# Kernel tuning notes

Measured on AMD Instinct MI355X. Metric: run time of the kernel, lower is better.

The kernel has to match this reference:

```python
import jax, jax.numpy as jnp
import numpy as np

B, S, H, HEADS = 4, 2048, 512, 8
DK = H // HEADS
LN_EPS = 1e-5
NEG_INF = -1e30


def setup_inputs() -> dict:
    key = jax.random.key(0)
    k = jax.random.split(key, 6)
    x = jax.random.normal(k[0], (B, S, H), dtype=jnp.float32)
    mask = jax.random.randint(k[1], (B, S), 0, 2, dtype=jnp.int32)
    # per-head Q/K/V projection weights stacked: [heads, H, dk]
    Wq = jax.random.normal(k[2], (HEADS, H, DK), dtype=jnp.float32) * 0.05
    Wk = jax.random.normal(k[3], (HEADS, H, DK), dtype=jnp.float32) * 0.05
    Wv = jax.random.normal(k[4], (HEADS, H, DK), dtype=jnp.float32) * 0.05
    # output projection: [heads*dk, H] (y = h @ Wo)
    Wo = jax.random.normal(k[5], (HEADS * DK, H), dtype=jnp.float32) * 0.05
    gamma = jnp.ones((H,), dtype=jnp.float32)
    beta = jnp.zeros((H,), dtype=jnp.float32)
    return {"x": x, "mask": mask, "Wq": Wq, "Wk": Wk, "Wv": Wv,
            "Wo": Wo, "gamma": gamma, "beta": beta}


def reference(x, mask, Wq, Wk, Wv, Wo, gamma, beta):
    # LayerNorm over hidden dim
    mu = jnp.mean(x, axis=-1, keepdims=True)
    var = jnp.mean(jnp.square(x - mu), axis=-1, keepdims=True)
    xn = (x - mu) * jax.lax.rsqrt(var + LN_EPS) * gamma + beta  # [B,S,H]

    mf = mask.astype(jnp.float32)  # [B,S]

    # batched per-head projections (original loops over heads)
    q = jnp.einsum('bsh,nhd->bnsd', xn, Wq)  # [B,heads,S,dk]
    kk = jnp.einsum('bsh,nhd->bnsd', xn, Wk)
    v = jnp.einsum('bsh,nhd->bnsd', xn, Wv)

    scores = jnp.einsum('bnqd,bnkd->bnqk', q, kk) / np.sqrt(DK).astype(np.float32)
    m = mf[:, None, None, :]  # [B,1,1,S] broadcast over query dim
    logits = m * scores + (1.0 - m) * NEG_INF
    probs = jax.nn.softmax(logits, axis=-1)
    attn = jnp.einsum('bnqk,bnkd->bnqd', probs, v)  # [B,heads,S,dk]

    h = attn.transpose(0, 2, 1, 3).reshape(x.shape[0], x.shape[1], HEADS * DK)
    out = h @ Wo + xn          # residual adds post-norm x (as in original)
    out = out * mf[:, :, None]  # zero out masked positions
    return out
```

## Files before the change

kernel.cpp:

```cpp
#include <hip/hip_runtime.h>
#include <hip/hip_bf16.h>
#include <math.h>

#define B_ 4
#define S_ 2048
#define H_ 512
#define HEADS_ 8
#define DK_ 64
#define NROWS_ (B_*S_)
#define LN_EPS_ 1e-5f
#define NEG_INF_ -1e30f
#define QSCALE_ (0.125f * 1.44269504088896f)

typedef short s8v __attribute__((ext_vector_type(8)));
typedef short s4v __attribute__((ext_vector_type(4)));
typedef float f4v __attribute__((ext_vector_type(4)));

__device__ __forceinline__ unsigned short f2bf(float f) {
    unsigned int u = __float_as_uint(f);
    u += 0x7FFFu + ((u >> 16) & 1u);
    return (unsigned short)(u >> 16);
}

__device__ __forceinline__ s4v pk4bf(float a, float b, float c, float d) {
    union { __hip_bfloat162 h[2]; s4v v; } u;
    u.h[0] = __float22bfloat162_rn(float2{a, b});
    u.h[1] = __float22bfloat162_rn(float2{c, d});
    return u.v;
}

__global__ __launch_bounds__(256) void wt_kernel(
        const float* __restrict__ Wq, const float* __restrict__ Wk,
        const float* __restrict__ Wv, const float* __restrict__ Wo,
        unsigned short* __restrict__ Wt) {
    __shared__ float tile[32][33];
    int z = blockIdx.z;
    int k0 = blockIdx.y * 32, c0 = blockIdx.x * 32;
    const float* src;
    int ld, drow;
    float scale = 1.f;
    if (z < 24) {
        if (blockIdx.x >= 2) return;
        int zw = z >> 3, head = z & 7;
        const float* W = (zw == 0) ? Wq : (zw == 1) ? Wk : Wv;
        if (zw == 0) scale = QSCALE_;
        src = W + (size_t)head * H_ * DK_;
        ld = DK_;
        drow = zw * 512 + head * 64;
    } else {
        src = Wo; ld = H_; drow = 1536;
    }
    int tx = threadIdx.x & 31, ty = threadIdx.x >> 5;
    #pragma unroll
    for (int i = 0; i < 4; i++)
        tile[ty * 4 + i][tx] = src[(size_t)(k0 + ty * 4 + i) * ld + c0 + tx];
    __syncthreads();
    #pragma unroll
    for (int i = 0; i < 4; i++) {
        int cc = ty * 4 + i;
        Wt[(size_t)(drow + c0 + cc) * 512 + k0 + tx] = f2bf(tile[tx][cc] * scale);
    }
}

__global__ __launch_bounds__(256) void ln_kernel(
        const float* __restrict__ x, const float* __restrict__ gamma,
        const float* __restrict__ beta, float* __restrict__ xn,
        unsigned short* __restrict__ xnb) {
    int row  = blockIdx.x * 4 + (threadIdx.x >> 6);
    int lane = threadIdx.x & 63;
    const float4* xr = (const float4*)(x + (size_t)row * H_ + lane * 8);
    float4 a = xr[0], d = xr[1];
    float s  = (a.x + a.y) + (a.z + a.w) + (d.x + d.y) + (d.z + d.w);
    float ss = (a.x*a.x + a.y*a.y) + (a.z*a.z + a.w*a.w)
             + (d.x*d.x + d.y*d.y) + (d.z*d.z + d.w*d.w);
    #pragma unroll
    for (int i = 1; i < 64; i <<= 1) {
        s  += __shfl_xor(s, i, 64);
        ss += __shfl_xor(ss, i, 64);
    }
    float mu  = s * (1.f / 512.f);
    float var = ss * (1.f / 512.f) - mu * mu;
    float rstd = rsqrtf(var + LN_EPS_);
    const float4* gp = (const float4*)(gamma + lane * 8);
    const float4* bp = (const float4*)(beta + lane * 8);
    float4 g0 = gp[0], g1 = gp[1], b0 = bp[0], b1 = bp[1];
    float4 y0, y1;
    y0.x = (a.x - mu) * rstd * g0.x + b0.x;
    y0.y = (a.y - mu) * rstd * g0.y + b0.y;
    y0.z = (a.z - mu) * rstd * g0.z + b0.z;
    y0.w = (a.w - mu) * rstd * g0.w + b0.w;
    y1.x = (d.x - mu) * rstd * g1.x + b1.x;
    y1.y = (d.y - mu) * rstd * g1.y + b1.y;
    y1.z = (d.z - mu) * rstd * g1.z + b1.z;
    y1.w = (d.w - mu) * rstd * g1.w + b1.w;
    float4* xo = (float4*)(xn + (size_t)row * H_ + lane * 8);
    xo[0] = y0; xo[1] = y1;
    union { s4v h[2]; s8v v; } pk;
    pk.h[0] = pk4bf(y0.x, y0.y, y0.z, y0.w);
    pk.h[1] = pk4bf(y1.x, y1.y, y1.z, y1.w);
    *(s8v*)(xnb + (size_t)row * H_ + lane * 8) = pk.v;
}

#define BK_ 32
__device__ __forceinline__ void gemm_tile(
        const unsigned short* __restrict__ A,
        const unsigned short* __restrict__ Bt,
        int r0, int j0, f4v acc[4][4]) {
    __shared__ unsigned short As[128][BK_ + 8];
    __shared__ unsigned short Bs[128][BK_ + 8];
    int t = threadIdx.x;
    int wv = t >> 6, L = t & 63, c = L & 15, g = L >> 4;
    int m_base = (wv & 1) * 64, n_base = (wv >> 1) * 64;
    #pragma unroll
    for (int i = 0; i < 4; i++)
        #pragma unroll
        for (int j = 0; j < 4; j++) acc[i][j] = (f4v){0.f, 0.f, 0.f, 0.f};
    for (int k0 = 0; k0 < 512; k0 += BK_) {
        __syncthreads();
        #pragma unroll
        for (int i = 0; i < 2; i++) {
            int idx = t + i * 256;
            int m = idx >> 2, k8 = idx & 3;
            s8v va = *(const s8v*)(A  + (size_t)(r0 + m) * 512 + k0 + k8 * 8);
            s8v vb = *(const s8v*)(Bt + (size_t)(j0 + m) * 512 + k0 + k8 * 8);
            *(s8v*)(&As[m][k8 * 8]) = va;
            *(s8v*)(&Bs[m][k8 * 8]) = vb;
        }
        __syncthreads();
        s8v a[4], b[4];
        #pragma unroll
        for (int i = 0; i < 4; i++)
            a[i] = *(const s8v*)(&As[m_base + i * 16 + c][g * 8]);
        #pragma unroll
        for (int j = 0; j < 4; j++)
            b[j] = *(const s8v*)(&Bs[n_base + j * 16 + c][g * 8]);
        #pragma unroll
        for (int i = 0; i < 4; i++)
            #pragma unroll
            for (int j = 0; j < 4; j++)
                acc[i][j] = __builtin_amdgcn_mfma_f32_16x16x32_bf16(
                    a[i], b[j], acc[i][j], 0, 0, 0);
    }
}

__global__ __launch_bounds__(256) void qkv_gemm(
        const unsigned short* __restrict__ xnb,
        const unsigned short* __restrict__ Wt,
        unsigned short* __restrict__ Qb, unsigned short* __restrict__ Kf,
        unsigned short* __restrict__ Vf) {
    f4v acc[4][4];
    int t = threadIdx.x;
    int wv = t >> 6, L = t & 63, c = L & 15, g = L >> 4;
    int rb = wv & 1, cb = wv >> 1;
    if (blockIdx.x < 8) {
        int m0 = blockIdx.x * 128, n0 = blockIdx.y * 128;
        gemm_tile(Wt, xnb, m0, n0, acc);
        int R0 = m0 + rb * 64;
        int C0 = n0 + cb * 64;
        int hd = (R0 >> 6) & 7;
        int b  = C0 >> 11, srow0 = C0 & 2047;
        size_t bhbase = (size_t)(b * HEADS_ + hd) * S_ * DK_;
        if (R0 < 512) {
            #pragma unroll
            for (int msub = 0; msub < 4; msub++) {
                int dk4 = msub * 16 + g * 4;
                #pragma unroll
                for (int nsub = 0; nsub < 4; nsub++) {
                    int tok = srow0 + nsub * 16 + c;
                    s4v v = pk4bf(acc[msub][nsub][0], acc[msub][nsub][1],
                                  acc[msub][nsub][2], acc[msub][nsub][3]);
                    *(s4v*)(Qb + bhbase + (size_t)tok * DK_ + dk4) = v;
                }
            }
        } else {
            unsigned short* dst = Kf + bhbase + (size_t)(srow0 >> 6) * 4096;
            #pragma unroll
            for (int msub = 0; msub < 4; msub++) {
                int gx = (msub & 1) * 2 + (g >> 1);
                int slotbase = (g & 1) * 4 + (msub >> 1) * 8;
                #pragma unroll
                for (int nsub = 0; nsub < 4; nsub++) {
                    s4v v = pk4bf(acc[msub][nsub][0], acc[msub][nsub][1],
                                  acc[msub][nsub][2], acc[msub][nsub][3]);
                    *(s4v*)(dst + nsub * 1024 + (gx * 16 + c) * 16 + slotbase) = v;
                }
            }
        }
    } else {
        int r0 = blockIdx.y * 128, j0 = 1024 + (blockIdx.x - 8) * 128;
        gemm_tile(xnb, Wt, r0, j0, acc);
        int R0 = r0 + rb * 64;
        int C0 = j0 + cb * 64;
        int hd = (C0 >> 6) & 7;
        int b = R0 >> 11, srow0 = R0 & 2047;
        unsigned short* dst = Vf + (size_t)(b * HEADS_ + hd) * S_ * DK_
                              + (size_t)(srow0 >> 6) * 4096;
        #pragma unroll
        for (int msub = 0; msub < 4; msub++)
            #pragma unroll
            for (int nsub = 0; nsub < 4; nsub++) {
                s4v v = pk4bf(acc[msub][nsub][0], acc[msub][nsub][1],
                              acc[msub][nsub][2], acc[msub][nsub][3]);
                *(s4v*)(dst + nsub * 1024 + (g * 16 + c) * 16 + msub * 4) = v;
            }
    }
}

__global__ __launch_bounds__(256, 3) void attn_kernel(
        const unsigned short* __restrict__ Qb,
        const unsigned short* __restrict__ Kf,
        const unsigned short* __restrict__ Vf,
        const int* __restrict__ mask,
        unsigned short* __restrict__ hb) {
    __shared__ float red[2][64][2][17];

    int wv   = threadIdx.x >> 6;
    int qsub = wv & 1;
    int kp   = wv >> 1;
    int L  = threadIdx.x & 63;
    int c  = L & 15;
    int g  = L >> 4;
    int bh = blockIdx.y;
    int b  = bh >> 3, n = bh & 7;
    int q0 = blockIdx.x * 64 + qsub * 32;

    const unsigned short* Qbase = Qb + (size_t)bh * S_ * DK_;
    const unsigned short* Kp = Kf + (size_t)bh * S_ * DK_ + (size_t)kp * 16 * 4096 + L * 16;
    const unsigned short* Vp = Vf + (size_t)bh * S_ * DK_ + (size_t)kp * 16 * 4096 + L * 16;
    const int* mrow = mask + b * S_ + kp * 1024;

    s8v qfA0 = *(const s8v*)(Qbase + (size_t)(q0 + c) * DK_ + g * 8);
    s8v qfA1 = *(const s8v*)(Qbase + (size_t)(q0 + c) * DK_ + 32 + g * 8);
    s8v qfB0 = *(const s8v*)(Qbase + (size_t)(q0 + 16 + c) * DK_ + g * 8);
    s8v qfB1 = *(const s8v*)(Qbase + (size_t)(q0 + 16 + c) * DK_ + 32 + g * 8);

    f4v accA[4], accB[4];
    #pragma unroll
    for (int i = 0; i < 4; i++) {
        accA[i] = (f4v){0.f, 0.f, 0.f, 0.f};
        accB[i] = (f4v){0.f, 0.f, 0.f, 0.f};
    }
    float lacA[4] = {0.f, 0.f, 0.f, 0.f};
    float lacB[4] = {0.f, 0.f, 0.f, 0.f};

    for (int kb = 0; kb < 16; kb++) {
        const unsigned short* Kn = Kp + (size_t)kb * 4096;
        const unsigned short* Vn = Vp + (size_t)kb * 4096;
        #pragma unroll
        for (int h = 0; h < 2; h++) {
            s8v k0lo = *(const s8v*)(Kn + (h * 2 + 0) * 1024);
            s8v k0hi = *(const s8v*)(Kn + (h * 2 + 0) * 1024 + 8);
            s8v k1lo = *(const s8v*)(Kn + (h * 2 + 1) * 1024);
            s8v k1hi = *(const s8v*)(Kn + (h * 2 + 1) * 1024 + 8);
            int4 mk0 = *(const int4*)(mrow + kb * 64 + h * 32 + g * 4);
            int4 mk1 = *(const int4*)(mrow + kb * 64 + h * 32 + 16 + g * 4);
            s8v vv[4];
            #pragma unroll
            for (int ds = 0; ds < 4; ds++)
                vv[ds] = *(const s8v*)(Vn + ds * 1024 + h * 8);
            f4v sA0 = (f4v){0.f,0.f,0.f,0.f}, sA1 = (f4v){0.f,0.f,0.f,0.f};
            f4v sB0 = (f4v){0.f,0.f,0.f,0.f}, sB1 = (f4v){0.f,0.f,0.f,0.f};
            sA0 = __builtin_amdgcn_mfma_f32_16x16x32_bf16(k0lo, qfA0, sA0, 0, 0, 0);
            sA0 = __builtin_amdgcn_mfma_f32_16x16x32_bf16(k0hi, qfA1, sA0, 0, 0, 0);
            sA1 = __builtin_amdgcn_mfma_f32_16x16x32_bf16(k1lo, qfA0, sA1, 0, 0, 0);
            sA1 = __builtin_amdgcn_mfma_f32_16x16x32_bf16(k1hi, qfA1, sA1, 0, 0, 0);
            sB0 = __builtin_amdgcn_mfma_f32_16x16x32_bf16(k0lo, qfB0, sB0, 0, 0, 0);
            sB0 = __builtin_amdgcn_mfma_f32_16x16x32_bf16(k0hi, qfB1, sB0, 0, 0, 0);
            sB1 = __builtin_amdgcn_mfma_f32_16x16x32_bf16(k1lo, qfB0, sB1, 0, 0, 0);
            sB1 = __builtin_amdgcn_mfma_f32_16x16x32_bf16(k1hi, qfB1, sB1, 0, 0, 0);
            float pA0[4], pA1[4], pB0[4], pB1[4];
            #pragma unroll
            for (int r = 0; r < 4; r++) {
                int m0 = (&mk0.x)[r], m1 = (&mk1.x)[r];
                pA0[r] = __builtin_amdgcn_exp2f(m0 ? sA0[r] : NEG_INF_);
                pA1[r] = __builtin_amdgcn_exp2f(m1 ? sA1[r] : NEG_INF_);
                pB0[r] = __builtin_amdgcn_exp2f(m0 ? sB0[r] : NEG_INF_);
                pB1[r] = __builtin_amdgcn_exp2f(m1 ? sB1[r] : NEG_INF_);
                lacA[r] += pA0[r] + pA1[r];
                lacB[r] += pB0[r] + pB1[r];
            }
            s4v pfA0 = pk4bf(pA0[0], pA0[1], pA0[2], pA0[3]);
            s4v pfA1 = pk4bf(pA1[0], pA1[1], pA1[2], pA1[3]);
            s4v pfB0 = pk4bf(pB0[0], pB0[1], pB0[2], pB0[3]);
            s4v pfB1 = pk4bf(pB1[0], pB1[1], pB1[2], pB1[3]);
            #pragma unroll
            for (int ds = 0; ds < 4; ds++) {
                s4v v0 = __builtin_shufflevector(vv[ds], vv[ds], 0, 1, 2, 3);
                s4v v1 = __builtin_shufflevector(vv[ds], vv[ds], 4, 5, 6, 7);
                accA[ds] = __builtin_amdgcn_mfma_f32_16x16x16bf16_1k(v0, pfA0, accA[ds], 0, 0, 0);
                accA[ds] = __builtin_amdgcn_mfma_f32_16x16x16bf16_1k(v1, pfA1, accA[ds], 0, 0, 0);
                accB[ds] = __builtin_amdgcn_mfma_f32_16x16x16bf16_1k(v0, pfB0, accB[ds], 0, 0, 0);
                accB[ds] = __builtin_amdgcn_mfma_f32_16x16x16bf16_1k(v1, pfB1, accB[ds], 0, 0, 0);
            }
        }
    }

    float lA = (lacA[0] + lacA[1]) + (lacA[2] + lacA[3]);
    float lB = (lacB[0] + lacB[1]) + (lacB[2] + lacB[3]);
    lA += __shfl_xor(lA, 16, 64);
    lA += __shfl_xor(lA, 32, 64);
    lB += __shfl_xor(lB, 16, 64);
    lB += __shfl_xor(lB, 32, 64);

    if (kp == 1) {
        #pragma unroll
        for (int d = 0; d < 4; d++) {
            #pragma unroll
            for (int r = 0; r < 4; r++) {
                red[qsub][L][0][d * 4 + r] = accA[d][r];
                red[qsub][L][1][d * 4 + r] = accB[d][r];
            }
        }
        red[qsub][L][0][16] = lA;
        red[qsub][L][1][16] = lB;
    }
    __syncthreads();
    if (kp == 0) {
        const float* srcA = &red[qsub][L][0][0];
        const float* srcB = &red[qsub][L][1][0];
        float invA = 1.f / (lA + srcA[16]);
        float invB = 1.f / (lB + srcB[16]);
        unsigned short* hpA = hb + (size_t)(b * S_ + q0 + c) * H_ + n * DK_ + g * 4;
        unsigned short* hpB = hpA + (size_t)16 * H_;
        #pragma unroll
        for (int ds = 0; ds < 4; ds++) {
            s4v oA = pk4bf((accA[ds][0] + srcA[ds * 4 + 0]) * invA,
                           (accA[ds][1] + srcA[ds * 4 + 1]) * invA,
                           (accA[ds][2] + srcA[ds * 4 + 2]) * invA,
                           (accA[ds][3] + srcA[ds * 4 + 3]) * invA);
            *(s4v*)(hpA + ds * 16) = oA;
            s4v oB = pk4bf((accB[ds][0] + srcB[ds * 4 + 0]) * invB,
                           (accB[ds][1] + srcB[ds * 4 + 1]) * invB,
                           (accB[ds][2] + srcB[ds * 4 + 2]) * invB,
                           (accB[ds][3] + srcB[ds * 4 + 3]) * invB);
            *(s4v*)(hpB + ds * 16) = oB;
        }
    }
}

__global__ __launch_bounds__(256) void out_gemm(
        const unsigned short* __restrict__ hb,
        const unsigned short* __restrict__ Wot,
        const float* __restrict__ xn, const int* __restrict__ mask,
        float* __restrict__ out) {
    f4v acc[4][4];
    int r0 = blockIdx.y * 128, j0 = blockIdx.x * 128;
    gemm_tile(hb, Wot, r0, j0, acc);
    int t = threadIdx.x;
    int wv = t >> 6, L = t & 63, c = L & 15, g = L >> 4;
    int mrow = r0 + (wv & 1) * 64 + g * 4;
    int ncol = j0 + (wv >> 1) * 64 + c;
    #pragma unroll
    for (int msub = 0; msub < 4; msub++) {
        #pragma unroll
        for (int rr = 0; rr < 4; rr++) {
            int row = mrow + msub * 16 + rr;
            float mf = (float)mask[row];
            #pragma unroll
            for (int nsub = 0; nsub < 4; nsub++) {
                int col = ncol + nsub * 16;
                size_t o = (size_t)row * H_ + col;
                out[o] = (acc[msub][nsub][rr] + xn[o]) * mf;
            }
        }
    }
}

extern "C" void kernel_launch(void* const* d_in, const int* in_sizes, int n_in,
                              void* d_out, int out_size, void* d_ws, size_t ws_size,
                              hipStream_t stream) {
    const float* x     = (const float*)d_in[0];
    const int*   mask  = (const int*)d_in[1];
    const float* Wq    = (const float*)d_in[2];
    const float* Wk    = (const float*)d_in[3];
    const float* Wv    = (const float*)d_in[4];
    const float* Wo    = (const float*)d_in[5];
    const float* gamma = (const float*)d_in[6];
    const float* beta  = (const float*)d_in[7];
    float* out = (float*)d_out;

    size_t nelem = (size_t)NROWS_ * H_;
    char* ws = (char*)d_ws;
    float*          xn  = (float*)ws;          ws += nelem * 4;
    unsigned short* xnb = (unsigned short*)ws; ws += nelem * 2;
    unsigned short* hb  = (unsigned short*)ws; ws += nelem * 2;
    unsigned short* Qb  = (unsigned short*)ws; ws += nelem * 2;
    unsigned short* Kf  = (unsigned short*)ws; ws += nelem * 2;
    unsigned short* Vf  = (unsigned short*)ws; ws += nelem * 2;
    unsigned short* Wt  = (unsigned short*)ws;

    wt_kernel<<<dim3(16, 16, 25), 256, 0, stream>>>(Wq, Wk, Wv, Wo, Wt);
    ln_kernel<<<NROWS_ / 4, 256, 0, stream>>>(x, gamma, beta, xn, xnb);
    qkv_gemm<<<dim3(12, 64), 256, 0, stream>>>(xnb, Wt, Qb, Kf, Vf);
    attn_kernel<<<dim3(S_ / 64, B_ * HEADS_), 256, 0, stream>>>(
        Qb, Kf, Vf, mask, hb);
    out_gemm<<<dim3(4, 64), 256, 0, stream>>>(
        hb, Wt + (size_t)1536 * 512, xn, mask, out);
}
```

Measured before the change: 194.6 us.

## Use direct global-to-LDS loads in GEMM tiles and fold mask into MFMA bias

The GEMM tile loader now uses global_load_lds to copy bf16 tiles straight into shared memory, so the data no longer passes through registers. The unpadded layout this requires may cause LDS bank conflicts on the fragment reads. The LayerNorm kernel also writes a per-key additive bias (0 or -1e30) derived from the mask. The attention kernel seeds the score accumulators with this bias, removing the per-element select before exp2.

Result: faster. 185.5 us (-4.7%).

```diff
diff --git a/kernel.cpp b/kernel.cpp
--- a/kernel.cpp
+++ b/kernel.cpp
@@ -15,6 +15,9 @@
 typedef short s8v __attribute__((ext_vector_type(8)));
 typedef short s4v __attribute__((ext_vector_type(4)));
 typedef float f4v __attribute__((ext_vector_type(4)));
+
+typedef __attribute__((address_space(1))) unsigned int gu32_t;
+typedef __attribute__((address_space(3))) unsigned int lu32_t;
 
 __device__ __forceinline__ unsigned short f2bf(float f) {
     unsigned int u = __float_as_uint(f);
@@ -64,8 +67,9 @@
 
 __global__ __launch_bounds__(256) void ln_kernel(
         const float* __restrict__ x, const float* __restrict__ gamma,
-        const float* __restrict__ beta, float* __restrict__ xn,
-        unsigned short* __restrict__ xnb) {
+        const float* __restrict__ beta, const int* __restrict__ mask,
+        float* __restrict__ xn, unsigned short* __restrict__ xnb,
+        float* __restrict__ mb) {
     int row  = blockIdx.x * 4 + (threadIdx.x >> 6);
     int lane = threadIdx.x & 63;
     const float4* xr = (const float4*)(x + (size_t)row * H_ + lane * 8);
@@ -81,6 +85,7 @@
     float mu  = s * (1.f / 512.f);
     float var = ss * (1.f / 512.f) - mu * mu;
     float rstd = rsqrtf(var + LN_EPS_);
+    if (lane == 0) mb[row] = mask[row] ? 0.f : NEG_INF_;
     const float4* gp = (const float4*)(gamma + lane * 8);
     const float4* bp = (const float4*)(beta + lane * 8);
     float4 g0 = gp[0], g1 = gp[1], b0 = bp[0], b1 = bp[1];
@@ -106,8 +111,8 @@
         const unsigned short* __restrict__ A,
         const unsigned short* __restrict__ Bt,
         int r0, int j0, f4v acc[4][4]) {
-    __shared__ unsigned short As[128][BK_ + 8];
-    __shared__ unsigned short Bs[128][BK_ + 8];
+    __shared__ unsigned short As[128 * BK_];
+    __shared__ unsigned short Bs[128 * BK_];
     int t = threadIdx.x;
     int wv = t >> 6, L = t & 63, c = L & 15, g = L >> 4;
     int m_base = (wv & 1) * 64, n_base = (wv >> 1) * 64;
@@ -119,21 +124,24 @@
         __syncthreads();
         #pragma unroll
         for (int i = 0; i < 2; i++) {
-            int idx = t + i * 256;
-            int m = idx >> 2, k8 = idx & 3;
-            s8v va = *(const s8v*)(A  + (size_t)(r0 + m) * 512 + k0 + k8 * 8);
-            s8v vb = *(const s8v*)(Bt + (size_t)(j0 + m) * 512 + k0 + k8 * 8);
-            *(s8v*)(&As[m][k8 * 8]) = va;
-            *(s8v*)(&Bs[m][k8 * 8]) = vb;
-        }
+            int u = wv * 128 + i * 64 + L;
+            int row = u >> 2, k8 = u & 3;
+            __builtin_amdgcn_global_load_lds(
+                (const gu32_t*)(A + (size_t)(r0 + row) * 512 + k0 + k8 * 8),
+                (lu32_t*)(As + (size_t)(wv * 128 + i * 64) * 8), 16, 0, 0);
+            __builtin_amdgcn_global_load_lds(
+                (const gu32_t*)(Bt + (size_t)(j0 + row) * 512 + k0 + k8 * 8),
+                (lu32_t*)(Bs + (size_t)(wv * 128 + i * 64) * 8), 16, 0, 0);
+        }
+        __asm__ volatile("s_waitcnt vmcnt(0)" ::: "memory");
         __syncthreads();
         s8v a[4], b[4];
         #pragma unroll
         for (int i = 0; i < 4; i++)
-            a[i] = *(const s8v*)(&As[m_base + i * 16 + c][g * 8]);
+            a[i] = *(const s8v*)(As + (size_t)(m_base + i * 16 + c) * BK_ + g * 8);
         #pragma unroll
         for (int j = 0; j < 4; j++)
-            b[j] = *(const s8v*)(&Bs[n_base + j * 16 + c][g * 8]);
+            b[j] = *(const s8v*)(Bs + (size_t)(n_base + j * 16 + c) * BK_ + g * 8);
         #pragma unroll
         for (int i = 0; i < 4; i++)
             #pragma unroll
@@ -210,7 +218,7 @@
         const unsigned short* __restrict__ Qb,
         const unsigned short* __restrict__ Kf,
         const unsigned short* __restrict__ Vf,
-        const int* __restrict__ mask,
+        const float* __restrict__ mb,
         unsigned short* __restrict__ hb) {
     __shared__ float red[2][64][2][17];
 
@@ -227,7 +235,7 @@
     const unsigned short* Qbase = Qb + (size_t)bh * S_ * DK_;
     const unsigned short* Kp = Kf + (size_t)bh * S_ * DK_ + (size_t)kp * 16 * 4096 + L * 16;
     const unsigned short* Vp = Vf + (size_t)bh * S_ * DK_ + (size_t)kp * 16 * 4096 + L * 16;
-    const int* mrow = mask + b * S_ + kp * 1024;
+    const float* mbrow = mb + b * S_ + kp * 1024;
 
     s8v qfA0 = *(const s8v*)(Qbase + (size_t)(q0 + c) * DK_ + g * 8);
     s8v qfA1 = *(const s8v*)(Qbase + (size_t)(q0 + c) * DK_ + 32 + g * 8);
@@ -252,14 +260,15 @@
             s8v k0hi = *(const s8v*)(Kn + (h * 2 + 0) * 1024 + 8);
             s8v k1lo = *(const s8v*)(Kn + (h * 2 + 1) * 1024);
             s8v k1hi = *(const s8v*)(Kn + (h * 2 + 1) * 1024 + 8);
-            int4 mk0 = *(const int4*)(mrow + kb * 64 + h * 32 + g * 4);
-            int4 mk1 = *(const int4*)(mrow + kb * 64 + h * 32 + 16 + g * 4);
+            float4 mb0 = *(const float4*)(mbrow + kb * 64 + h * 32 + g * 4);
+            float4 mb1 = *(const float4*)(mbrow + kb * 64 + h * 32 + 16 + g * 4);
             s8v vv[4];
             #pragma unroll
             for (int ds = 0; ds < 4; ds++)
                 vv[ds] = *(const s8v*)(Vn + ds * 1024 + h * 8);
-            f4v sA0 = (f4v){0.f,0.f,0.f,0.f}, sA1 = (f4v){0.f,0.f,0.f,0.f};
-            f4v sB0 = (f4v){0.f,0.f,0.f,0.f}, sB1 = (f4v){0.f,0.f,0.f,0.f};
+            f4v bias0 = (f4v){mb0.x, mb0.y, mb0.z, mb0.w};
+            f4v bias1 = (f4v){mb1.x, mb1.y, mb1.z, mb1.w};
+            f4v sA0 = bias0, sA1 = bias1, sB0 = bias0, sB1 = bias1;
             sA0 = __builtin_amdgcn_mfma_f32_16x16x32_bf16(k0lo, qfA0, sA0, 0, 0, 0);
             sA0 = __builtin_amdgcn_mfma_f32_16x16x32_bf16(k0hi, qfA1, sA0, 0, 0, 0);
             sA1 = __builtin_amdgcn_mfma_f32_16x16x32_bf16(k1lo, qfA0, sA1, 0, 0, 0);
@@ -271,11 +280,10 @@
             float pA0[4], pA1[4], pB0[4], pB1[4];
             #pragma unroll
             for (int r = 0; r < 4; r++) {
-                int m0 = (&mk0.x)[r], m1 = (&mk1.x)[r];
-                pA0[r] = __builtin_amdgcn_exp2f(m0 ? sA0[r] : NEG_INF_);
-                pA1[r] = __builtin_amdgcn_exp2f(m1 ? sA1[r] : NEG_INF_);
-                pB0[r] = __builtin_amdgcn_exp2f(m0 ? sB0[r] : NEG_INF_);
-                pB1[r] = __builtin_amdgcn_exp2f(m1 ? sB1[r] : NEG_INF_);
+                pA0[r] = __builtin_amdgcn_exp2f(sA0[r]);
+                pA1[r] = __builtin_amdgcn_exp2f(sA1[r]);
+                pB0[r] = __builtin_amdgcn_exp2f(sB0[r]);
+                pB1[r] = __builtin_amdgcn_exp2f(sB1[r]);
                 lacA[r] += pA0[r] + pA1[r];
                 lacB[r] += pB0[r] + pB1[r];
             }
@@ -387,13 +395,14 @@
     unsigned short* Qb  = (unsigned short*)ws; ws += nelem * 2;
     unsigned short* Kf  = (unsigned short*)ws; ws += nelem * 2;
     unsigned short* Vf  = (unsigned short*)ws; ws += nelem * 2;
-    unsigned short* Wt  = (unsigned short*)ws;
+    unsigned short* Wt  = (unsigned short*)ws; ws += (size_t)2048 * 512 * 2;
+    float*          mbp = (float*)ws;
 
     wt_kernel<<<dim3(16, 16, 25), 256, 0, stream>>>(Wq, Wk, Wv, Wo, Wt);
-    ln_kernel<<<NROWS_ / 4, 256, 0, stream>>>(x, gamma, beta, xn, xnb);
+    ln_kernel<<<NROWS_ / 4, 256, 0, stream>>>(x, gamma, beta, mask, xn, xnb, mbp);
     qkv_gemm<<<dim3(12, 64), 256, 0, stream>>>(xnb, Wt, Qb, Kf, Vf);
     attn_kernel<<<dim3(S_ / 64, B_ * HEADS_), 256, 0, stream>>>(
-        Qb, Kf, Vf, mask, hb);
+        Qb, Kf, Vf, mbp, hb);
     out_gemm<<<dim3(4, 64), 256, 0, stream>>>(
         hb, Wt + (size_t)1536 * 512, xn, mask, out);
 }
```
